# Optimization experiments

Hardware: AMD Instinct MI355X
Metric: run time of the kernel (lower is better)

The kernel has to match this reference:

```python
import jax, jax.numpy as jnp
import numpy as np

M, D, NI, L, NPL, R, T = 2, 128, 131072, 4, 2048, 8, 32
N = NI + L * NPL  # total DAG nodes


def setup_inputs() -> dict:
    key = jax.random.key(0)
    ks = jax.random.split(key, 18)
    thax = jax.random.randint(ks[0], (NI,), 0, T)
    sine = jax.random.uniform(ks[1], (NI,), jnp.float32)
    # parents of layer-l deriv nodes index any node built earlier (topological)
    raw = jax.random.randint(ks[2], (L, NPL, 2), 0, 2**30)
    bounds = jnp.array([NI + l * NPL for l in range(L)])[:, None, None]
    par = raw % bounds
    ridx = jax.random.randint(ks[3], (L, NPL), 0, R)
    pos = jax.random.uniform(ks[4], (N,), jnp.float32) + 0.01
    neg = jax.random.uniform(ks[5], (N,), jnp.float32) + 0.01
    s = 0.05
    return {
        'thax': thax, 'sine': sine, 'par': par, 'ridx': ridx,
        'pos': pos, 'neg': neg,
        'init_table': jax.random.normal(ks[6], (M, T, D)) * s,
        's_vec': jax.random.normal(ks[7], (M, D)) * s,
        'W1': jax.random.normal(ks[8], (M, R, 2 * D, D)) * s,
        'b1': jax.random.normal(ks[9], (M, R, D)) * s,
        'W2': jax.random.normal(ks[10], (M, R, D, D)) * s,
        'b2': jax.random.normal(ks[11], (M, R, D)) * s,
        'tweaks': jax.random.normal(ks[12], (M, 1, 2)) * s,
        'We1': jax.random.normal(ks[13], (M, D, D)) * s,
        'be1': jax.random.normal(ks[14], (M, D)) * s,
        'we2': jax.random.normal(ks[15], (M, D)) * s,
        'be2': jax.random.normal(ks[16], (M,)) * s,
    }


def reference(thax, sine, par, ridx, pos, neg, init_table, s_vec,
              W1, b1, W2, b2, tweaks, We1, be1, we2, be2):
    # init nodes: thax embedding + sine embellishment (per model)
    emb0 = init_table[:, thax, :] + sine[None, :, None] * s_vec[:, None, :]  # [M,NI,D]
    store = jnp.zeros((M, N, D), emb0.dtype).at[:, :NI].set(emb0)
    # topological layers of deriv nodes: gather parents, rule-indexed 2-layer MLP
    for l in range(L):
        p, r = par[l], ridx[l]
        cat = store[:, p].reshape(M, NPL, 2 * D)               # gather parents
        h = jax.nn.relu(jnp.einsum('mnc,mncd->mnd', cat, W1[:, r]) + b1[:, r])
        out = (jnp.einsum('mnd,mnde->mne', h, W2[:, r]) + b2[:, r]
               + tweaks[:, 0, 1][:, None, None])
        store = store.at[:, NI + l * NPL: NI + (l + 1) * NPL].set(out)
    # eval_net: per-node scalar logit (+ per-problem tweak)
    he = jax.nn.relu(jnp.einsum('mnd,mde->mne', store, We1) + be1[:, None, :])
    logit = jnp.einsum('mnd,md->mn', he, we2) + be2[:, None] + tweaks[:, 0, 0][:, None]
    tot_pos, tot_neg = pos.sum(), neg.sum()
    pw = tot_neg / tot_pos  # POS_WEIGHT_EXTRA = 1.0
    gold = pos / (pos + neg)
    w = pos + neg
    # BCEWithLogitsLoss(pos_weight=pw) per node, weighted by (pos+neg)
    bce = -(pw * gold[None] * jax.nn.log_sigmoid(logit)
            + (1.0 - gold[None]) * jax.nn.log_sigmoid(-logit))
    loss = (w[None] * bce).sum(axis=1)                          # [M]
    posOK = jnp.where(logit >= 0, pos[None], 0.0).sum(axis=1)
    negOK = jnp.where(logit < 0, neg[None], 0.0).sum(axis=1)
    return (loss, posOK, negOK, tot_pos, tot_neg)
```

## Files before the change

kernel.cpp:

```cpp
#include <hip/hip_runtime.h>
#include <hip/hip_bf16.h>

#define M_ 2
#define D_ 128
#define NI_ 131072
#define L_ 4
#define NPL_ 2048
#define R_ 8
#define T_ 32
#define N_ (NI_ + L_ * NPL_)
#define ND_ (L_ * NPL_)
#define PART2_ 1184

typedef __bf16 bf16x8 __attribute__((ext_vector_type(8)));
typedef float f32x4 __attribute__((ext_vector_type(4)));

#define OFF_W1T    0u
#define OFF_W2T    1048576u
#define OFF_WE1T   1572864u
#define OFF_TAB    1638400u
#define OFF_SVEC   1654784u
#define OFF_SORTED 1655296u
#define OFF_STARTS 1688064u
#define OFF_CNTF   1688192u
#define OFF_CNTA   1688320u
#define OFF_EA2    1688448u
#define OFF_EWB    1721216u
#define OFF_PA     1723264u
#define OFF_PB     1739648u
#define OFF_PPOK   1756032u
#define OFF_PNOK   1772416u
#define OFF_PTP    1788800u
#define OFF_PTN    1805184u
#define OFF_G      1821568u
#define OFF_STORE  2362240u
#define OFF_FSG    6556544u
#define OFF_CFG    6556576u
#define OFF_FLIST  6556608u
#define OFF_RDY    6589376u

__device__ __forceinline__ unsigned short f2bu(float f) {
  unsigned int u = __float_as_uint(f);
  u += 0x7fffu + ((u >> 16) & 1u);
  return (unsigned short)(u >> 16);
}
__device__ __forceinline__ bf16x8 ldb8(const unsigned short* p) {
  return *reinterpret_cast<const bf16x8*>(p);
}

__device__ __forceinline__ bf16x8 node_chunk(int m, int row, int d0,
    const unsigned short* tab, const unsigned short* svec,
    const unsigned short* sd, const int* thax, const float* sine) {
  if (row < NI_) {
    bf16x8 tv = ldb8(&tab[(m * T_ + thax[row]) * D_ + d0]);
    bf16x8 sv = ldb8(&svec[m * D_ + d0]);
    float sn = sine[row];
    bf16x8 r;
#pragma unroll
    for (int j = 0; j < 8; ++j)
      r[j] = (__bf16)((float)tv[j] + sn * (float)sv[j]);
    return r;
  }
  return ldb8(&sd[(size_t)(m * ND_ + (row - NI_)) * D_ + d0]);
}

__global__ __launch_bounds__(256) void megaprep_kernel(
    const float* W1, const float* W2, const float* We1,
    const float* init_table, const float* s_vec,
    const float* b1, const float* be1, const float* we2,
    const int* ridx, const int* par,
    unsigned short* W1T, unsigned short* W2T, unsigned short* We1T,
    unsigned short* tab, unsigned short* svec,
    float* G, float* EA2, float* EWB,
    int* sorted, int* starts, int* cntF, int* cntA,
    int* fsg, int* cfg, int* fastlist, unsigned int* rdy, unsigned int* pzero) {
  __shared__ float smem[1056];
  __shared__ int icnt[16], ioff[16];
  int job = blockIdx.x;
  int tid = threadIdx.x;

  if (job < 800) {
    int z, rblk, cblk;
    if (job < 512)      { z = job >> 5;            rblk = (job & 31) >> 2; cblk = job & 3; }
    else if (job < 768) { int q = job - 512; z = 16 + (q >> 4); rblk = (q & 15) >> 2; cblk = q & 3; }
    else                { int q = job - 768; z = 32 + (q >> 4); rblk = (q & 15) >> 2; cblk = q & 3; }
    const float* src; unsigned short* dst; int R;
    if (z < 16)      { src = W1  + (size_t)z * 32768;        dst = W1T  + (size_t)z * 32768;        R = 256; }
    else if (z < 32) { src = W2  + (size_t)(z - 16) * 16384; dst = W2T  + (size_t)(z - 16) * 16384; R = 128; }
    else             { src = We1 + (size_t)(z - 32) * 16384; dst = We1T + (size_t)(z - 32) * 16384; R = 128; }
    int r0 = rblk * 32, c0 = cblk * 32;
    float (*tile)[33] = (float(*)[33])smem;
    int tx = tid & 31, ty = tid >> 5;
#pragma unroll
    for (int k = 0; k < 4; ++k)
      tile[ty + 8 * k][tx] = src[(size_t)(r0 + ty + 8 * k) * D_ + c0 + tx];
    __syncthreads();
#pragma unroll
    for (int k = 0; k < 4; ++k)
      dst[(size_t)(c0 + ty + 8 * k) * R + r0 + tx] = f2bu(tile[tx][ty + 8 * k]);
  } else if (job == 800) {
    for (int i = tid; i < 8448; i += 256) {
      if (i < 8192) tab[i] = f2bu(init_table[i]);
      else svec[i - 8192] = f2bu(s_vec[i - 8192]);
    }
  } else if (job < 1329) {
    int q = job - 801;
    int t = q / 16, mr = q & 15;
    int m = mr >> 3;
    int slot = tid >> 7, e = tid & 127;
    const float* vec = (t < 32) ? &init_table[(size_t)(m * T_ + t) * D_]
                                : &s_vec[(size_t)m * D_];
    if (tid < 128) smem[tid] = vec[tid];
    __syncthreads();
    const float* w = &W1[((size_t)mr * 256 + slot * 128) * D_];
    float acc = 0.f;
#pragma unroll 8
    for (int c = 0; c < 128; ++c) acc = fmaf(smem[c], w[c * D_ + e], acc);
    if (slot == 0 && t < 32) acc += b1[mr * D_ + e];
    G[((size_t)(mr * 2 + slot) * 33 + t) * D_ + e] = acc;
  } else if (job < 1363) {
    int q = job - 1329;
    int m = q / 17, t = (q % 17) * 2 + (tid >> 7);
    int e = tid & 127;
    if (t <= 32) {
      const float* vec = (t < 32) ? &init_table[(size_t)(m * T_ + t) * D_]
                                  : &s_vec[(size_t)m * D_];
      const float* w = &We1[(size_t)m * D_ * D_];
      float acc = 0.f;
#pragma unroll 8
      for (int d = 0; d < 128; ++d) acc = fmaf(vec[d], w[d * D_ + e], acc);
      if (t < 32) {
        EA2[m * 4096 + ((e >> 1) * 32 + t) * 2 + (e & 1)] = acc + be1[m * D_ + e];
      } else {
        EWB[(m * D_ + e) * 2 + 0] = acc;
        EWB[(m * D_ + e) * 2 + 1] = we2[m * D_ + e];
      }
    }
  } else if (job < 1367) {
    int l = job - 1363;
    if (tid < 16) icnt[tid] = 0;
    __syncthreads();
    for (int n = tid; n < NPL_; n += 256) {
      int r = ridx[l * NPL_ + n];
      int p0 = par[(l * NPL_ + n) * 2 + 0], p1 = par[(l * NPL_ + n) * 2 + 1];
      int slow = (p0 >= NI_ || p1 >= NI_) ? 1 : 0;
      atomicAdd(&icnt[r * 2 + slow], 1);
    }
    __syncthreads();
    if (tid == 0) {
      int run = 0;
      for (int b = 0; b < 16; ++b) { ioff[b] = run; run += icnt[b]; }
      for (int r = 0; r < R_; ++r) {
        starts[l * R_ + r] = ioff[2 * r];
        cntF[l * R_ + r] = icnt[2 * r];
        cntA[l * R_ + r] = icnt[2 * r] + icnt[2 * r + 1];
      }
    }
    __syncthreads();
    for (int n = tid; n < NPL_; n += 256) {
      int r = ridx[l * NPL_ + n];
      int p0 = par[(l * NPL_ + n) * 2 + 0], p1 = par[(l * NPL_ + n) * 2 + 1];
      int slow = (p0 >= NI_ || p1 >= NI_) ? 1 : 0;
      int p = atomicAdd(&ioff[r * 2 + slow], 1);
      sorted[l * NPL_ + p] = n;
    }
  } else if (job == 1367) {
    if (tid < 8) icnt[tid] = 0;
    __syncthreads();
    for (int g = tid; g < ND_; g += 256) {
      int p0 = par[2 * g], p1 = par[2 * g + 1];
      int fast = (p0 < NI_ && p1 < NI_) ? 1 : 0;
      if (fast) atomicAdd(&icnt[ridx[g]], 1);
      rdy[g] = fast ? 2u : 0u;
      rdy[ND_ + g] = fast ? 2u : 0u;
    }
    __syncthreads();
    if (tid == 0) {
      int run = 0;
      for (int r = 0; r < R_; ++r) {
        ioff[r] = run; fsg[r] = run; cfg[r] = icnt[r]; run += icnt[r];
      }
    }
    __syncthreads();
    for (int g = tid; g < ND_; g += 256) {
      int p0 = par[2 * g], p1 = par[2 * g + 1];
      if (p0 < NI_ && p1 < NI_) {
        int p = atomicAdd(&ioff[ridx[g]], 1);
        fastlist[p] = g;
      }
    }
  } else {
    for (int i = tid; i < 24576; i += 256) pzero[i] = 0u;
  }
}

__global__ __launch_bounds__(256) void main_kernel(
    const int* thax, const float* sine, const int* par,
    const float* pos, const float* neg,
    const float* b2, const float* tweaks,
    const float* G, const unsigned short* W2T, const unsigned short* We1T,
    const float* EA2, const float* EWB,
    const float* be1, const float* we2, const float* be2,
    const int* fsg, const int* cfg, const int* fastlist,
    unsigned short* sd,
    float* pA, float* pB, float* pPok, float* pNok, float* pTp, float* pTn) {
  __shared__ float sbuf[4448];
  int bid = blockIdx.x;
  int tid = threadIdx.x;
  int w = tid >> 6, lane = tid & 63;

  if (bid < 1280) {
    int m = bid / 640, q = bid % 640;
    int r = q / 80, tile = q % 80;
    int cnt = cfg[r];
    int base = tile * 16;
    if (base >= cnt) return;
    unsigned short* h_lds = (unsigned short*)sbuf;
    int*   t0a  = (int*)(sbuf + 1024);
    int*   t1a  = t0a + 16;
    float* s0a  = (float*)(t1a + 16);
    float* s1a  = s0a + 16;
    int*   gida = (int*)(s1a + 16);
    float* red2 = sbuf + 1104;
    if (tid < 16) {
      int loc = base + tid; if (loc >= cnt) loc = cnt - 1;
      int gid = fastlist[fsg[r] + loc];
      int p0 = par[2 * gid], p1 = par[2 * gid + 1];
      t0a[tid] = thax[p0]; s0a[tid] = sine[p0];
      t1a[tid] = thax[p1]; s1a[tid] = sine[p1];
      gida[tid] = gid;
    }
    __syncthreads();
    const float* Gm = &G[(size_t)(m * R_ + r) * 8448];
    {
      int row = tid >> 4, seg = tid & 15, d0 = seg * 8;
      int t0 = t0a[row], t1 = t1a[row];
      float s0 = s0a[row], s1 = s1a[row];
      const float* pa = &Gm[t0 * 128 + d0];
      const float* pb = &Gm[(33 + t1) * 128 + d0];
      const float* pu = &Gm[4096 + d0];
      const float* pv = &Gm[8320 + d0];
      bf16x8 hv;
#pragma unroll
      for (int half = 0; half < 2; ++half) {
        float4 a = *(const float4*)(pa + half * 4);
        float4 b = *(const float4*)(pb + half * 4);
        float4 u = *(const float4*)(pu + half * 4);
        float4 v = *(const float4*)(pv + half * 4);
        hv[half * 4 + 0] = (__bf16)fmaxf(a.x + b.x + s0 * u.x + s1 * v.x, 0.f);
        hv[half * 4 + 1] = (__bf16)fmaxf(a.y + b.y + s0 * u.y + s1 * v.y, 0.f);
        hv[half * 4 + 2] = (__bf16)fmaxf(a.z + b.z + s0 * u.z + s1 * v.z, 0.f);
        hv[half * 4 + 3] = (__bf16)fmaxf(a.w + b.w + s0 * u.w + s1 * v.w, 0.f);
      }
      *(bf16x8*)&h_lds[row * 128 + (d0 ^ ((row & 7) << 3))] = hv;
    }
    __syncthreads();
    int l15 = lane & 15, l4 = lane >> 4;
    const unsigned short* w2b = &W2T[(size_t)(m * R_ + r) * D_ * D_];
    f32x4 acc[2];
    acc[0] = (f32x4){0.f, 0.f, 0.f, 0.f};
    acc[1] = (f32x4){0.f, 0.f, 0.f, 0.f};
#pragma unroll
    for (int kc = 0; kc < 4; ++kc) {
      int d0 = kc * 32 + l4 * 8;
      bf16x8 a2 = ldb8(&h_lds[l15 * 128 + (d0 ^ ((l15 & 7) << 3))]);
#pragma unroll
      for (int f = 0; f < 2; ++f) {
        int fg = w * 2 + f;
        bf16x8 b = ldb8(&w2b[(fg * 16 + l15) * D_ + d0]);
        acc[f] = __builtin_amdgcn_mfma_f32_16x16x32_bf16(a2, b, acc[f], 0, 0, 0);
      }
    }
    float tw1 = tweaks[m * 2 + 1];
    const float* b2v = &b2[(m * R_ + r) * D_];
    __syncthreads();
#pragma unroll
    for (int i = 0; i < 4; ++i) {
      int row = l4 * 4 + i;
      int g = base + row;
#pragma unroll
      for (int f = 0; f < 2; ++f) {
        int e = (w * 2 + f) * 16 + l15;
        unsigned short val = f2bu(acc[f][i] + b2v[e] + tw1);
        h_lds[row * 128 + (e ^ ((row & 7) << 3))] = val;
        if (g < cnt) sd[(size_t)(m * ND_ + gida[row]) * D_ + e] = val;
      }
    }
    __syncthreads();
    f32x4 ae[2];
    ae[0] = (f32x4){0.f, 0.f, 0.f, 0.f};
    ae[1] = (f32x4){0.f, 0.f, 0.f, 0.f};
    const unsigned short* we1b = &We1T[(size_t)m * D_ * D_];
#pragma unroll
    for (int kc = 0; kc < 4; ++kc) {
      int d0 = kc * 32 + l4 * 8;
      bf16x8 a2 = ldb8(&h_lds[l15 * 128 + (d0 ^ ((l15 & 7) << 3))]);
#pragma unroll
      for (int f = 0; f < 2; ++f) {
        int fg = w * 2 + f;
        bf16x8 b = ldb8(&we1b[(fg * 16 + l15) * D_ + d0]);
        ae[f] = __builtin_amdgcn_mfma_f32_16x16x32_bf16(a2, b, ae[f], 0, 0, 0);
      }
    }
    float part[4] = {0.f, 0.f, 0.f, 0.f};
#pragma unroll
    for (int f = 0; f < 2; ++f) {
      int e = (w * 2 + f) * 16 + l15;
      float bb = be1[m * D_ + e];
      float wv = we2[m * D_ + e];
#pragma unroll
      for (int i = 0; i < 4; ++i) {
        float he = ae[f][i] + bb;
        he = he > 0.f ? he : 0.f;
        part[i] += he * wv;
      }
    }
#pragma unroll
    for (int mask = 1; mask < 16; mask <<= 1) {
#pragma unroll
      for (int i = 0; i < 4; ++i) part[i] += __shfl_xor(part[i], mask, 64);
    }
    if (l15 == 0) {
#pragma unroll
      for (int i = 0; i < 4; ++i) red2[w * 16 + l4 * 4 + i] = part[i];
    }
    __syncthreads();
    if (tid < 16) {
      int g = base + tid;
      float v6[6] = {0.f, 0.f, 0.f, 0.f, 0.f, 0.f};
      if (g < cnt) {
        float logit = red2[tid] + red2[16 + tid] + red2[32 + tid] + red2[48 + tid]
                    + be2[m] + tweaks[m * 2 + 0];
        int grow = NI_ + gida[tid];
        float p_ = pos[grow], n_ = neg[grow];
        float lse = log1pf(__expf(-fabsf(logit)));
        v6[0] = p_ * (fmaxf(-logit, 0.f) + lse);
        v6[1] = n_ * (fmaxf(logit, 0.f) + lse);
        v6[2] = logit >= 0.f ? p_ : 0.f;
        v6[3] = logit < 0.f ? n_ : 0.f;
        v6[4] = p_; v6[5] = n_;
      }
#pragma unroll
      for (int mask = 1; mask < 16; mask <<= 1) {
#pragma unroll
        for (int qq = 0; qq < 6; ++qq) v6[qq] += __shfl_xor(v6[qq], mask, 64);
      }
      if (tid == 0) {
        int slot = 512 + r * 80 + tile;
        pA[m * PART2_ + slot] = v6[0];
        pB[m * PART2_ + slot] = v6[1];
        pPok[m * PART2_ + slot] = v6[2];
        pNok[m * PART2_ + slot] = v6[3];
        if (m == 0) { pTp[slot] = v6[4]; pTn[slot] = v6[5]; }
      }
    }
  } else {
    int q = bid - 1280;
    int m = q >> 9, xb = q & 511;
    float* lea = sbuf;
    float* lwb = sbuf + 4096;
    float* red = sbuf + 4352;
    for (int i = tid; i < 4096; i += 256) lea[i] = EA2[m * 4096 + i];
    if (tid < 256) lwb[tid] = EWB[m * 256 + tid];
    __syncthreads();
    int row = xb * 256 + tid;
    int t = thax[row];
    float s = sine[row];
    float acc = 0.f;
#pragma unroll 8
    for (int p = 0; p < 64; ++p) {
      float2 ea = *(const float2*)&lea[(p * 32 + t) * 2];
      float4 wb = *(const float4*)&lwb[p * 4];
      float x0 = fmaf(s, wb.x, ea.x); x0 = fmaxf(x0, 0.f);
      acc = fmaf(x0, wb.y, acc);
      float x1 = fmaf(s, wb.z, ea.y); x1 = fmaxf(x1, 0.f);
      acc = fmaf(x1, wb.w, acc);
    }
    float logit = acc + be2[m] + tweaks[m * 2 + 0];
    float p_ = pos[row], n_ = neg[row];
    float lse = log1pf(__expf(-fabsf(logit)));
    float v[6];
    v[0] = p_ * (fmaxf(-logit, 0.f) + lse);
    v[1] = n_ * (fmaxf(logit, 0.f) + lse);
    v[2] = logit >= 0.f ? p_ : 0.f;
    v[3] = logit < 0.f ? n_ : 0.f;
    v[4] = p_; v[5] = n_;
#pragma unroll
    for (int mask = 1; mask < 64; mask <<= 1) {
#pragma unroll
      for (int k = 0; k < 6; ++k) v[k] += __shfl_xor(v[k], mask, 64);
    }
    if (lane == 0) {
#pragma unroll
      for (int k = 0; k < 6; ++k) red[k * 16 + w] = v[k];
    }
    __syncthreads();
    if (tid == 0) {
      float t6[6];
#pragma unroll
      for (int k = 0; k < 6; ++k)
        t6[k] = red[k * 16 + 0] + red[k * 16 + 1] + red[k * 16 + 2] + red[k * 16 + 3];
      pA[m * PART2_ + xb] = t6[0];
      pB[m * PART2_ + xb] = t6[1];
      pPok[m * PART2_ + xb] = t6[2];
      pNok[m * PART2_ + xb] = t6[3];
      if (m == 0) { pTp[xb] = t6[4]; pTn[xb] = t6[5]; }
    }
  }
}

__global__ __launch_bounds__(256) void slowfused_kernel(
    const int* thax, const float* sine, const int* par,
    const float* b1, const float* b2, const float* tweaks,
    const float* pos, const float* neg,
    const float* be1, const float* we2, const float* be2,
    const unsigned short* tab, const unsigned short* svec,
    const unsigned short* W1T, const unsigned short* W2T,
    const unsigned short* We1T,
    const int* sorted, const int* starts, const int* cntF, const int* cntA,
    unsigned short* sd, unsigned int* rdy,
    float* pA, float* pB, float* pPok, float* pNok, float* pTp, float* pTn) {
  __shared__ unsigned short h_lds[16 * 128];
  __shared__ float red2[64];
  __shared__ float pacc[6];
  __shared__ int sfl;
  int bid = blockIdx.x;
  int m = bid >> 5, r = (bid >> 2) & 7, ts = bid & 3;
  int tid = threadIdx.x;
  int w = tid >> 6, lane = tid & 63;
  int l15 = lane & 15, l4 = lane >> 4;
  if (tid < 6) pacc[tid] = 0.f;
  float tw1 = tweaks[m * 2 + 1];
  const float* b2v = &b2[(m * R_ + r) * D_];
  const unsigned short* w1b = &W1T[(size_t)(m * R_ + r) * D_ * 256];
  const unsigned short* w2b = &W2T[(size_t)(m * R_ + r) * D_ * D_];
  const unsigned short* we1b = &We1T[(size_t)m * D_ * D_];

  for (int l = 1; l < L_; ++l) {
    int cF = cntF[l * R_ + r];
    int cS = cntA[l * R_ + r] - cF;
    int base = ts * 16;
    if (base < cS) {
      int start = starts[l * R_ + r] + cF;
      if (tid == 0) sfl = 0;
      __syncthreads();
      if (tid < 32) {
        int row = tid >> 1, which = tid & 1;
        int loc = base + row; if (loc >= cS) loc = cS - 1;
        int node = sorted[l * NPL_ + start + loc];
        int p = par[(l * NPL_ + node) * 2 + which];
        if (p >= NI_) {
          unsigned int* fp = &rdy[(size_t)m * ND_ + (p - NI_)];
          unsigned int v = __hip_atomic_load(fp, __ATOMIC_ACQUIRE, __HIP_MEMORY_SCOPE_AGENT);
          int spins = 0;
          while (v == 0 && spins < (1 << 17)) {
            __builtin_amdgcn_s_sleep(8);
            v = __hip_atomic_load(fp, __ATOMIC_ACQUIRE, __HIP_MEMORY_SCOPE_AGENT);
            ++spins;
          }
          if (v != 2u) atomicOr(&sfl, 1);
        }
      }
      __syncthreads();
      if (sfl && tid == 0) __threadfence();
      __syncthreads();
      int loc = base + l15; if (loc >= cS) loc = cS - 1;
      int node = sorted[l * NPL_ + start + loc];
      int p0 = par[(l * NPL_ + node) * 2 + 0];
      int p1 = par[(l * NPL_ + node) * 2 + 1];
      bf16x8 av[8];
#pragma unroll
      for (int kc = 0; kc < 8; ++kc) {
        int k = kc * 32 + l4 * 8;
        int p = (k < 128) ? p0 : p1;
        av[kc] = node_chunk(m, p, k & 127, tab, svec, sd, thax, sine);
      }
      f32x4 acch[2];
      acch[0] = (f32x4){0.f, 0.f, 0.f, 0.f};
      acch[1] = (f32x4){0.f, 0.f, 0.f, 0.f};
#pragma unroll
      for (int kc = 0; kc < 8; ++kc) {
        int k = kc * 32 + l4 * 8;
#pragma unroll
        for (int f = 0; f < 2; ++f) {
          int fg = w * 2 + f;
          bf16x8 b = ldb8(&w1b[(fg * 16 + l15) * 256 + k]);
          acch[f] = __builtin_amdgcn_mfma_f32_16x16x32_bf16(av[kc], b, acch[f], 0, 0, 0);
        }
      }
      const float* b1v = &b1[(m * R_ + r) * D_];
#pragma unroll
      for (int f = 0; f < 2; ++f) {
        int d = (w * 2 + f) * 16 + l15;
        float bb = b1v[d];
#pragma unroll
        for (int i = 0; i < 4; ++i) {
          int row = l4 * 4 + i;
          float h = acch[f][i] + bb;
          h = h > 0.f ? h : 0.f;
          h_lds[row * 128 + (d ^ ((row & 7) << 3))] = f2bu(h);
        }
      }
      __syncthreads();
      f32x4 acco[2];
      acco[0] = (f32x4){0.f, 0.f, 0.f, 0.f};
      acco[1] = (f32x4){0.f, 0.f, 0.f, 0.f};
#pragma unroll
      for (int kc = 0; kc < 4; ++kc) {
        int d0 = kc * 32 + l4 * 8;
        bf16x8 a2 = ldb8(&h_lds[l15 * 128 + (d0 ^ ((l15 & 7) << 3))]);
#pragma unroll
        for (int f = 0; f < 2; ++f) {
          int fg = w * 2 + f;
          bf16x8 b = ldb8(&w2b[(fg * 16 + l15) * D_ + d0]);
          acco[f] = __builtin_amdgcn_mfma_f32_16x16x32_bf16(a2, b, acco[f], 0, 0, 0);
        }
      }
      __syncthreads();
#pragma unroll
      for (int i = 0; i < 4; ++i) {
        int row = l4 * 4 + i;
        int g = base + row;
#pragma unroll
        for (int f = 0; f < 2; ++f) {
          int e = (w * 2 + f) * 16 + l15;
          unsigned short val = f2bu(acco[f][i] + b2v[e] + tw1);
          h_lds[row * 128 + (e ^ ((row & 7) << 3))] = val;
          if (g < cS) {
            int nd = sorted[l * NPL_ + start + g];
            sd[(size_t)(m * ND_ + l * NPL_ + nd) * D_ + e] = val;
          }
        }
      }
      __syncthreads();
      if (tid == 0) __threadfence();
      __syncthreads();
      if (tid < 16) {
        int g = base + tid;
        if (g < cS) {
          int nd = sorted[l * NPL_ + start + g];
          __hip_atomic_store(&rdy[(size_t)m * ND_ + l * NPL_ + nd], 1u,
                             __ATOMIC_RELAXED, __HIP_MEMORY_SCOPE_AGENT);
        }
      }
      f32x4 ae[2];
      ae[0] = (f32x4){0.f, 0.f, 0.f, 0.f};
      ae[1] = (f32x4){0.f, 0.f, 0.f, 0.f};
#pragma unroll
      for (int kc = 0; kc < 4; ++kc) {
        int d0 = kc * 32 + l4 * 8;
        bf16x8 a2 = ldb8(&h_lds[l15 * 128 + (d0 ^ ((l15 & 7) << 3))]);
#pragma unroll
        for (int f = 0; f < 2; ++f) {
          int fg = w * 2 + f;
          bf16x8 b = ldb8(&we1b[(fg * 16 + l15) * D_ + d0]);
          ae[f] = __builtin_amdgcn_mfma_f32_16x16x32_bf16(a2, b, ae[f], 0, 0, 0);
        }
      }
      float part[4] = {0.f, 0.f, 0.f, 0.f};
#pragma unroll
      for (int f = 0; f < 2; ++f) {
        int e = (w * 2 + f) * 16 + l15;
        float bb = be1[m * D_ + e];
        float wv = we2[m * D_ + e];
#pragma unroll
        for (int i = 0; i < 4; ++i) {
          float he = ae[f][i] + bb;
          he = he > 0.f ? he : 0.f;
          part[i] += he * wv;
        }
      }
#pragma unroll
      for (int mask = 1; mask < 16; mask <<= 1) {
#pragma unroll
        for (int i = 0; i < 4; ++i) part[i] += __shfl_xor(part[i], mask, 64);
      }
      if (l15 == 0) {
#pragma unroll
        for (int i = 0; i < 4; ++i) red2[w * 16 + l4 * 4 + i] = part[i];
      }
      __syncthreads();
      if (tid < 16) {
        int g = base + tid;
        float v6[6] = {0.f, 0.f, 0.f, 0.f, 0.f, 0.f};
        if (g < cS) {
          float logit = red2[tid] + red2[16 + tid] + red2[32 + tid] + red2[48 + tid]
                      + be2[m] + tweaks[m * 2 + 0];
          int nd = sorted[l * NPL_ + start + g];
          int grow = NI_ + l * NPL_ + nd;
          float p_ = pos[grow], n_ = neg[grow];
          float lse = log1pf(__expf(-fabsf(logit)));
          v6[0] = p_ * (fmaxf(-logit, 0.f) + lse);
          v6[1] = n_ * (fmaxf(logit, 0.f) + lse);
          v6[2] = logit >= 0.f ? p_ : 0.f;
          v6[3] = logit < 0.f ? n_ : 0.f;
          v6[4] = p_; v6[5] = n_;
        }
#pragma unroll
        for (int mask = 1; mask < 16; mask <<= 1) {
#pragma unroll
          for (int qq = 0; qq < 6; ++qq) v6[qq] += __shfl_xor(v6[qq], mask, 64);
        }
        if (tid == 0) {
#pragma unroll
          for (int qq = 0; qq < 6; ++qq) pacc[qq] += v6[qq];
        }
      }
      __syncthreads();
    }
  }
  if (tid == 0) {
    int slot = 1152 + (r * 4 + ts);
    pA[m * PART2_ + slot] = pacc[0];
    pB[m * PART2_ + slot] = pacc[1];
    pPok[m * PART2_ + slot] = pacc[2];
    pNok[m * PART2_ + slot] = pacc[3];
    if (m == 0) { pTp[slot] = pacc[4]; pTn[slot] = pacc[5]; }
  }
}

__global__ __launch_bounds__(256) void finalize_kernel(
    const float* pA, const float* pB, const float* pPok, const float* pNok,
    const float* pTp, const float* pTn, float* out) {
  __shared__ float lred[10][4];
  const float* srcs[10] = {pA, pA + PART2_, pB, pB + PART2_,
                           pPok, pPok + PART2_, pNok, pNok + PART2_,
                           pTp, pTn};
  int tid = threadIdx.x;
  int w = tid >> 6, lane = tid & 63;
#pragma unroll
  for (int q = 0; q < 10; ++q) {
    float s = 0.f;
    for (int i = tid; i < PART2_; i += 256) s += srcs[q][i];
#pragma unroll
    for (int mask = 1; mask < 64; mask <<= 1) s += __shfl_xor(s, mask, 64);
    if (lane == 0) lred[q][w] = s;
  }
  __syncthreads();
  if (tid == 0) {
    float totals[10];
#pragma unroll
    for (int q = 0; q < 10; ++q)
      totals[q] = lred[q][0] + lred[q][1] + lred[q][2] + lred[q][3];
    float tp = totals[8], tn = totals[9];
    float pw = tn / tp;
    out[0] = pw * totals[0] + totals[2];
    out[1] = pw * totals[1] + totals[3];
    out[2] = totals[4]; out[3] = totals[5];
    out[4] = totals[6]; out[5] = totals[7];
    out[6] = tp; out[7] = tn;
  }
}

extern "C" void kernel_launch(void* const* d_in, const int* in_sizes, int n_in,
                              void* d_out, int out_size, void* d_ws, size_t ws_size,
                              hipStream_t stream) {
  const int*   thax = (const int*)d_in[0];
  const float* sine = (const float*)d_in[1];
  const int*   par  = (const int*)d_in[2];
  const int*   ridx = (const int*)d_in[3];
  const float* pos  = (const float*)d_in[4];
  const float* neg  = (const float*)d_in[5];
  const float* init_table = (const float*)d_in[6];
  const float* s_vec = (const float*)d_in[7];
  const float* W1 = (const float*)d_in[8];
  const float* b1 = (const float*)d_in[9];
  const float* W2 = (const float*)d_in[10];
  const float* b2 = (const float*)d_in[11];
  const float* tweaks = (const float*)d_in[12];
  const float* We1 = (const float*)d_in[13];
  const float* be1 = (const float*)d_in[14];
  const float* we2 = (const float*)d_in[15];
  const float* be2 = (const float*)d_in[16];

  char* ws = (char*)d_ws;
  unsigned short* W1T  = (unsigned short*)(ws + OFF_W1T);
  unsigned short* W2T  = (unsigned short*)(ws + OFF_W2T);
  unsigned short* We1T = (unsigned short*)(ws + OFF_WE1T);
  unsigned short* tab  = (unsigned short*)(ws + OFF_TAB);
  unsigned short* svec = (unsigned short*)(ws + OFF_SVEC);
  int* sorted = (int*)(ws + OFF_SORTED);
  int* starts = (int*)(ws + OFF_STARTS);
  int* cntF   = (int*)(ws + OFF_CNTF);
  int* cntA   = (int*)(ws + OFF_CNTA);
  float* EA2  = (float*)(ws + OFF_EA2);
  float* EWB  = (float*)(ws + OFF_EWB);
  float* pA   = (float*)(ws + OFF_PA);
  float* pB   = (float*)(ws + OFF_PB);
  float* pPok = (float*)(ws + OFF_PPOK);
  float* pNok = (float*)(ws + OFF_PNOK);
  float* pTp  = (float*)(ws + OFF_PTP);
  float* pTn  = (float*)(ws + OFF_PTN);
  float* G    = (float*)(ws + OFF_G);
  unsigned short* sd = (unsigned short*)(ws + OFF_STORE);
  int* fsg      = (int*)(ws + OFF_FSG);
  int* cfg      = (int*)(ws + OFF_CFG);
  int* fastlist = (int*)(ws + OFF_FLIST);
  unsigned int* rdy = (unsigned int*)(ws + OFF_RDY);

  megaprep_kernel<<<1369, 256, 0, stream>>>(
      W1, W2, We1, init_table, s_vec, b1, be1, we2, ridx, par,
      W1T, W2T, We1T, tab, svec, G, EA2, EWB, sorted, starts, cntF, cntA,
      fsg, cfg, fastlist, rdy, (unsigned int*)pA);
  main_kernel<<<2304, 256, 0, stream>>>(
      thax, sine, par, pos, neg, b2, tweaks, G, W2T, We1T, EA2, EWB,
      be1, we2, be2, fsg, cfg, fastlist, sd,
      pA, pB, pPok, pNok, pTp, pTn);
  slowfused_kernel<<<64, 256, 0, stream>>>(
      thax, sine, par, b1, b2, tweaks, pos, neg, be1, we2, be2,
      tab, svec, W1T, W2T, We1T, sorted, starts, cntF, cntA,
      sd, rdy, pA, pB, pPok, pNok, pTp, pTn);
  finalize_kernel<<<1, 256, 0, stream>>>(pA, pB, pPok, pNok, pTp, pTn,
                                         (float*)d_out);
}
```

Before: 102.1 us.

## Replace spin-wait ready flags with per-layer kernel launches for slow nodes

The persistent slow-path kernel, which used per-node ready flags with acquire spin loops to enforce cross-layer dependencies, is replaced by three launches of a slow-node kernel, one per layer (layers 1-3). Each launch uses a grid of 8 tiles by 8 rules by 2 models with 128-thread blocks, and each wave computes four 16-column groups. This removes the rdy array initialization, the spin polling and the fences, and lets the launch boundary provide the ordering. The cost is two extra kernel launches, and each layer now runs with a fixed grid in which blocks past the slow-node count exit early.

```diff
diff --git a/kernel.cpp b/kernel.cpp
--- a/kernel.cpp
+++ b/kernel.cpp
@@ -10,7 +10,7 @@
 #define T_ 32
 #define N_ (NI_ + L_ * NPL_)
 #define ND_ (L_ * NPL_)
-#define PART2_ 1184
+#define PART3_ 1344
 
 typedef __bf16 bf16x8 __attribute__((ext_vector_type(8)));
 typedef float f32x4 __attribute__((ext_vector_type(4)));
@@ -27,17 +27,16 @@
 #define OFF_EA2    1688448u
 #define OFF_EWB    1721216u
 #define OFF_PA     1723264u
-#define OFF_PB     1739648u
-#define OFF_PPOK   1756032u
-#define OFF_PNOK   1772416u
-#define OFF_PTP    1788800u
-#define OFF_PTN    1805184u
-#define OFF_G      1821568u
-#define OFF_STORE  2362240u
-#define OFF_FSG    6556544u
-#define OFF_CFG    6556576u
-#define OFF_FLIST  6556608u
-#define OFF_RDY    6589376u
+#define OFF_PB     1734016u
+#define OFF_PPOK   1744768u
+#define OFF_PNOK   1755520u
+#define OFF_PTP    1766272u
+#define OFF_PTN    1771648u
+#define OFF_G      1777024u
+#define OFF_STORE  2317696u
+#define OFF_FSG    6512000u
+#define OFF_CFG    6512032u
+#define OFF_FLIST  6512064u
 
 __device__ __forceinline__ unsigned short f2bu(float f) {
   unsigned int u = __float_as_uint(f);
@@ -73,7 +72,7 @@
     unsigned short* tab, unsigned short* svec,
     float* G, float* EA2, float* EWB,
     int* sorted, int* starts, int* cntF, int* cntA,
-    int* fsg, int* cfg, int* fastlist, unsigned int* rdy, unsigned int* pzero) {
+    int* fsg, int* cfg, int* fastlist, unsigned int* pzero) {
   __shared__ float smem[1056];
   __shared__ int icnt[16], ioff[16];
   int job = blockIdx.x;
@@ -169,10 +168,7 @@
     __syncthreads();
     for (int g = tid; g < ND_; g += 256) {
       int p0 = par[2 * g], p1 = par[2 * g + 1];
-      int fast = (p0 < NI_ && p1 < NI_) ? 1 : 0;
-      if (fast) atomicAdd(&icnt[ridx[g]], 1);
-      rdy[g] = fast ? 2u : 0u;
-      rdy[ND_ + g] = fast ? 2u : 0u;
+      if (p0 < NI_ && p1 < NI_) atomicAdd(&icnt[ridx[g]], 1);
     }
     __syncthreads();
     if (tid == 0) {
@@ -190,7 +186,7 @@
       }
     }
   } else {
-    for (int i = tid; i < 24576; i += 256) pzero[i] = 0u;
+    for (int i = tid; i < 13440; i += 256) pzero[i] = 0u;
   }
 }
 
@@ -347,10 +343,10 @@
       }
       if (tid == 0) {
         int slot = 512 + r * 80 + tile;
-        pA[m * PART2_ + slot] = v6[0];
-        pB[m * PART2_ + slot] = v6[1];
-        pPok[m * PART2_ + slot] = v6[2];
-        pNok[m * PART2_ + slot] = v6[3];
+        pA[m * PART3_ + slot] = v6[0];
+        pB[m * PART3_ + slot] = v6[1];
+        pPok[m * PART3_ + slot] = v6[2];
+        pNok[m * PART3_ + slot] = v6[3];
         if (m == 0) { pTp[slot] = v6[4]; pTn[slot] = v6[5]; }
       }
     }
@@ -400,16 +396,16 @@
 #pragma unroll
       for (int k = 0; k < 6; ++k)
         t6[k] = red[k * 16 + 0] + red[k * 16 + 1] + red[k * 16 + 2] + red[k * 16 + 3];
-      pA[m * PART2_ + xb] = t6[0];
-      pB[m * PART2_ + xb] = t6[1];
-      pPok[m * PART2_ + xb] = t6[2];
-      pNok[m * PART2_ + xb] = t6[3];
+      pA[m * PART3_ + xb] = t6[0];
+      pB[m * PART3_ + xb] = t6[1];
+      pPok[m * PART3_ + xb] = t6[2];
+      pNok[m * PART3_ + xb] = t6[3];
       if (m == 0) { pTp[xb] = t6[4]; pTn[xb] = t6[5]; }
     }
   }
 }
 
-__global__ __launch_bounds__(256) void slowfused_kernel(
+__global__ __launch_bounds__(128) void slow_eval_kernel(int l,
     const int* thax, const float* sine, const int* par,
     const float* b1, const float* b2, const float* tweaks,
     const float* pos, const float* neg,
@@ -418,204 +414,160 @@
     const unsigned short* W1T, const unsigned short* W2T,
     const unsigned short* We1T,
     const int* sorted, const int* starts, const int* cntF, const int* cntA,
-    unsigned short* sd, unsigned int* rdy,
+    unsigned short* sd,
     float* pA, float* pB, float* pPok, float* pNok, float* pTp, float* pTn) {
-  __shared__ unsigned short h_lds[16 * 128];
-  __shared__ float red2[64];
-  __shared__ float pacc[6];
-  __shared__ int sfl;
-  int bid = blockIdx.x;
-  int m = bid >> 5, r = (bid >> 2) & 7, ts = bid & 3;
+  int tile = blockIdx.x, r = blockIdx.y, m = blockIdx.z;
+  int cF = cntF[l * R_ + r];
+  int cS = cntA[l * R_ + r] - cF;
+  int base = tile * 16;
+  if (base >= cS) return;
+  int start = starts[l * R_ + r] + cF;
   int tid = threadIdx.x;
   int w = tid >> 6, lane = tid & 63;
   int l15 = lane & 15, l4 = lane >> 4;
-  if (tid < 6) pacc[tid] = 0.f;
-  float tw1 = tweaks[m * 2 + 1];
-  const float* b2v = &b2[(m * R_ + r) * D_];
+  __shared__ unsigned short h_lds[16 * 128];
+  __shared__ float red2[32];
+
+  int loc = base + l15; if (loc >= cS) loc = cS - 1;
+  int node = sorted[l * NPL_ + start + loc];
+  int p0 = par[(l * NPL_ + node) * 2 + 0];
+  int p1 = par[(l * NPL_ + node) * 2 + 1];
   const unsigned short* w1b = &W1T[(size_t)(m * R_ + r) * D_ * 256];
   const unsigned short* w2b = &W2T[(size_t)(m * R_ + r) * D_ * D_];
   const unsigned short* we1b = &We1T[(size_t)m * D_ * D_];
 
-  for (int l = 1; l < L_; ++l) {
-    int cF = cntF[l * R_ + r];
-    int cS = cntA[l * R_ + r] - cF;
-    int base = ts * 16;
-    if (base < cS) {
-      int start = starts[l * R_ + r] + cF;
-      if (tid == 0) sfl = 0;
-      __syncthreads();
-      if (tid < 32) {
-        int row = tid >> 1, which = tid & 1;
-        int loc = base + row; if (loc >= cS) loc = cS - 1;
-        int node = sorted[l * NPL_ + start + loc];
-        int p = par[(l * NPL_ + node) * 2 + which];
-        if (p >= NI_) {
-          unsigned int* fp = &rdy[(size_t)m * ND_ + (p - NI_)];
-          unsigned int v = __hip_atomic_load(fp, __ATOMIC_ACQUIRE, __HIP_MEMORY_SCOPE_AGENT);
-          int spins = 0;
-          while (v == 0 && spins < (1 << 17)) {
-            __builtin_amdgcn_s_sleep(8);
-            v = __hip_atomic_load(fp, __ATOMIC_ACQUIRE, __HIP_MEMORY_SCOPE_AGENT);
-            ++spins;
-          }
-          if (v != 2u) atomicOr(&sfl, 1);
-        }
-      }
-      __syncthreads();
-      if (sfl && tid == 0) __threadfence();
-      __syncthreads();
-      int loc = base + l15; if (loc >= cS) loc = cS - 1;
-      int node = sorted[l * NPL_ + start + loc];
-      int p0 = par[(l * NPL_ + node) * 2 + 0];
-      int p1 = par[(l * NPL_ + node) * 2 + 1];
-      bf16x8 av[8];
-#pragma unroll
-      for (int kc = 0; kc < 8; ++kc) {
-        int k = kc * 32 + l4 * 8;
-        int p = (k < 128) ? p0 : p1;
-        av[kc] = node_chunk(m, p, k & 127, tab, svec, sd, thax, sine);
-      }
-      f32x4 acch[2];
-      acch[0] = (f32x4){0.f, 0.f, 0.f, 0.f};
-      acch[1] = (f32x4){0.f, 0.f, 0.f, 0.f};
-#pragma unroll
-      for (int kc = 0; kc < 8; ++kc) {
-        int k = kc * 32 + l4 * 8;
-#pragma unroll
-        for (int f = 0; f < 2; ++f) {
-          int fg = w * 2 + f;
-          bf16x8 b = ldb8(&w1b[(fg * 16 + l15) * 256 + k]);
-          acch[f] = __builtin_amdgcn_mfma_f32_16x16x32_bf16(av[kc], b, acch[f], 0, 0, 0);
-        }
-      }
-      const float* b1v = &b1[(m * R_ + r) * D_];
-#pragma unroll
-      for (int f = 0; f < 2; ++f) {
-        int d = (w * 2 + f) * 16 + l15;
-        float bb = b1v[d];
-#pragma unroll
-        for (int i = 0; i < 4; ++i) {
-          int row = l4 * 4 + i;
-          float h = acch[f][i] + bb;
-          h = h > 0.f ? h : 0.f;
-          h_lds[row * 128 + (d ^ ((row & 7) << 3))] = f2bu(h);
-        }
-      }
-      __syncthreads();
-      f32x4 acco[2];
-      acco[0] = (f32x4){0.f, 0.f, 0.f, 0.f};
-      acco[1] = (f32x4){0.f, 0.f, 0.f, 0.f};
-#pragma unroll
-      for (int kc = 0; kc < 4; ++kc) {
-        int d0 = kc * 32 + l4 * 8;
-        bf16x8 a2 = ldb8(&h_lds[l15 * 128 + (d0 ^ ((l15 & 7) << 3))]);
-#pragma unroll
-        for (int f = 0; f < 2; ++f) {
-          int fg = w * 2 + f;
-          bf16x8 b = ldb8(&w2b[(fg * 16 + l15) * D_ + d0]);
-          acco[f] = __builtin_amdgcn_mfma_f32_16x16x32_bf16(a2, b, acco[f], 0, 0, 0);
-        }
-      }
-      __syncthreads();
-#pragma unroll
-      for (int i = 0; i < 4; ++i) {
-        int row = l4 * 4 + i;
-        int g = base + row;
-#pragma unroll
-        for (int f = 0; f < 2; ++f) {
-          int e = (w * 2 + f) * 16 + l15;
-          unsigned short val = f2bu(acco[f][i] + b2v[e] + tw1);
-          h_lds[row * 128 + (e ^ ((row & 7) << 3))] = val;
-          if (g < cS) {
-            int nd = sorted[l * NPL_ + start + g];
-            sd[(size_t)(m * ND_ + l * NPL_ + nd) * D_ + e] = val;
-          }
-        }
-      }
-      __syncthreads();
-      if (tid == 0) __threadfence();
-      __syncthreads();
-      if (tid < 16) {
-        int g = base + tid;
-        if (g < cS) {
-          int nd = sorted[l * NPL_ + start + g];
-          __hip_atomic_store(&rdy[(size_t)m * ND_ + l * NPL_ + nd], 1u,
-                             __ATOMIC_RELAXED, __HIP_MEMORY_SCOPE_AGENT);
-        }
-      }
-      f32x4 ae[2];
-      ae[0] = (f32x4){0.f, 0.f, 0.f, 0.f};
-      ae[1] = (f32x4){0.f, 0.f, 0.f, 0.f};
-#pragma unroll
-      for (int kc = 0; kc < 4; ++kc) {
-        int d0 = kc * 32 + l4 * 8;
-        bf16x8 a2 = ldb8(&h_lds[l15 * 128 + (d0 ^ ((l15 & 7) << 3))]);
-#pragma unroll
-        for (int f = 0; f < 2; ++f) {
-          int fg = w * 2 + f;
-          bf16x8 b = ldb8(&we1b[(fg * 16 + l15) * D_ + d0]);
-          ae[f] = __builtin_amdgcn_mfma_f32_16x16x32_bf16(a2, b, ae[f], 0, 0, 0);
-        }
-      }
-      float part[4] = {0.f, 0.f, 0.f, 0.f};
-#pragma unroll
-      for (int f = 0; f < 2; ++f) {
-        int e = (w * 2 + f) * 16 + l15;
-        float bb = be1[m * D_ + e];
-        float wv = we2[m * D_ + e];
-#pragma unroll
-        for (int i = 0; i < 4; ++i) {
-          float he = ae[f][i] + bb;
-          he = he > 0.f ? he : 0.f;
-          part[i] += he * wv;
-        }
-      }
-#pragma unroll
-      for (int mask = 1; mask < 16; mask <<= 1) {
-#pragma unroll
-        for (int i = 0; i < 4; ++i) part[i] += __shfl_xor(part[i], mask, 64);
-      }
-      if (l15 == 0) {
-#pragma unroll
-        for (int i = 0; i < 4; ++i) red2[w * 16 + l4 * 4 + i] = part[i];
-      }
-      __syncthreads();
-      if (tid < 16) {
-        int g = base + tid;
-        float v6[6] = {0.f, 0.f, 0.f, 0.f, 0.f, 0.f};
-        if (g < cS) {
-          float logit = red2[tid] + red2[16 + tid] + red2[32 + tid] + red2[48 + tid]
-                      + be2[m] + tweaks[m * 2 + 0];
-          int nd = sorted[l * NPL_ + start + g];
-          int grow = NI_ + l * NPL_ + nd;
-          float p_ = pos[grow], n_ = neg[grow];
-          float lse = log1pf(__expf(-fabsf(logit)));
-          v6[0] = p_ * (fmaxf(-logit, 0.f) + lse);
-          v6[1] = n_ * (fmaxf(logit, 0.f) + lse);
-          v6[2] = logit >= 0.f ? p_ : 0.f;
-          v6[3] = logit < 0.f ? n_ : 0.f;
-          v6[4] = p_; v6[5] = n_;
-        }
-#pragma unroll
-        for (int mask = 1; mask < 16; mask <<= 1) {
-#pragma unroll
-          for (int qq = 0; qq < 6; ++qq) v6[qq] += __shfl_xor(v6[qq], mask, 64);
-        }
-        if (tid == 0) {
-#pragma unroll
-          for (int qq = 0; qq < 6; ++qq) pacc[qq] += v6[qq];
-        }
-      }
-      __syncthreads();
-    }
-  }
-  if (tid == 0) {
-    int slot = 1152 + (r * 4 + ts);
-    pA[m * PART2_ + slot] = pacc[0];
-    pB[m * PART2_ + slot] = pacc[1];
-    pPok[m * PART2_ + slot] = pacc[2];
-    pNok[m * PART2_ + slot] = pacc[3];
-    if (m == 0) { pTp[slot] = pacc[4]; pTn[slot] = pacc[5]; }
+  bf16x8 av[8];
+#pragma unroll
+  for (int kc = 0; kc < 8; ++kc) {
+    int k = kc * 32 + l4 * 8;
+    int p = (k < 128) ? p0 : p1;
+    av[kc] = node_chunk(m, p, k & 127, tab, svec, sd, thax, sine);
+  }
+  f32x4 acch[4];
+#pragma unroll
+  for (int f = 0; f < 4; ++f) acch[f] = (f32x4){0.f, 0.f, 0.f, 0.f};
+#pragma unroll
+  for (int kc = 0; kc < 8; ++kc) {
+    int k = kc * 32 + l4 * 8;
+#pragma unroll
+    for (int f = 0; f < 4; ++f) {
+      int fg = w * 4 + f;
+      bf16x8 b = ldb8(&w1b[(fg * 16 + l15) * 256 + k]);
+      acch[f] = __builtin_amdgcn_mfma_f32_16x16x32_bf16(av[kc], b, acch[f], 0, 0, 0);
+    }
+  }
+  const float* b1v = &b1[(m * R_ + r) * D_];
+#pragma unroll
+  for (int f = 0; f < 4; ++f) {
+    int d = (w * 4 + f) * 16 + l15;
+    float bb = b1v[d];
+#pragma unroll
+    for (int i = 0; i < 4; ++i) {
+      int row = l4 * 4 + i;
+      float h = acch[f][i] + bb;
+      h = h > 0.f ? h : 0.f;
+      h_lds[row * 128 + (d ^ ((row & 7) << 3))] = f2bu(h);
+    }
+  }
+  __syncthreads();
+  f32x4 acco[4];
+#pragma unroll
+  for (int f = 0; f < 4; ++f) acco[f] = (f32x4){0.f, 0.f, 0.f, 0.f};
+#pragma unroll
+  for (int kc = 0; kc < 4; ++kc) {
+    int d0 = kc * 32 + l4 * 8;
+    bf16x8 a2 = ldb8(&h_lds[l15 * 128 + (d0 ^ ((l15 & 7) << 3))]);
+#pragma unroll
+    for (int f = 0; f < 4; ++f) {
+      int fg = w * 4 + f;
+      bf16x8 b = ldb8(&w2b[(fg * 16 + l15) * D_ + d0]);
+      acco[f] = __builtin_amdgcn_mfma_f32_16x16x32_bf16(a2, b, acco[f], 0, 0, 0);
+    }
+  }
+  float tw1 = tweaks[m * 2 + 1];
+  const float* b2v = &b2[(m * R_ + r) * D_];
+  __syncthreads();
+#pragma unroll
+  for (int i = 0; i < 4; ++i) {
+    int row = l4 * 4 + i;
+    int g = base + row;
+#pragma unroll
+    for (int f = 0; f < 4; ++f) {
+      int e = (w * 4 + f) * 16 + l15;
+      unsigned short val = f2bu(acco[f][i] + b2v[e] + tw1);
+      h_lds[row * 128 + (e ^ ((row & 7) << 3))] = val;
+      if (g < cS) {
+        int nd = sorted[l * NPL_ + start + g];
+        sd[(size_t)(m * ND_ + l * NPL_ + nd) * D_ + e] = val;
+      }
+    }
+  }
+  __syncthreads();
+  f32x4 ae[4];
+#pragma unroll
+  for (int f = 0; f < 4; ++f) ae[f] = (f32x4){0.f, 0.f, 0.f, 0.f};
+#pragma unroll
+  for (int kc = 0; kc < 4; ++kc) {
+    int d0 = kc * 32 + l4 * 8;
+    bf16x8 a2 = ldb8(&h_lds[l15 * 128 + (d0 ^ ((l15 & 7) << 3))]);
+#pragma unroll
+    for (int f = 0; f < 4; ++f) {
+      int fg = w * 4 + f;
+      bf16x8 b = ldb8(&we1b[(fg * 16 + l15) * D_ + d0]);
+      ae[f] = __builtin_amdgcn_mfma_f32_16x16x32_bf16(a2, b, ae[f], 0, 0, 0);
+    }
+  }
+  float part[4] = {0.f, 0.f, 0.f, 0.f};
+#pragma unroll
+  for (int f = 0; f < 4; ++f) {
+    int e = (w * 4 + f) * 16 + l15;
+    float bb = be1[m * D_ + e];
+    float wv = we2[m * D_ + e];
+#pragma unroll
+    for (int i = 0; i < 4; ++i) {
+      float he = ae[f][i] + bb;
+      he = he > 0.f ? he : 0.f;
+      part[i] += he * wv;
+    }
+  }
+#pragma unroll
+  for (int mask = 1; mask < 16; mask <<= 1) {
+#pragma unroll
+    for (int i = 0; i < 4; ++i) part[i] += __shfl_xor(part[i], mask, 64);
+  }
+  if (l15 == 0) {
+#pragma unroll
+    for (int i = 0; i < 4; ++i) red2[w * 16 + l4 * 4 + i] = part[i];
+  }
+  __syncthreads();
+  if (tid < 16) {
+    int g = base + tid;
+    float v6[6] = {0.f, 0.f, 0.f, 0.f, 0.f, 0.f};
+    if (g < cS) {
+      float logit = red2[tid] + red2[16 + tid] + be2[m] + tweaks[m * 2 + 0];
+      int nd = sorted[l * NPL_ + start + g];
+      int grow = NI_ + l * NPL_ + nd;
+      float p_ = pos[grow], n_ = neg[grow];
+      float lse = log1pf(__expf(-fabsf(logit)));
+      v6[0] = p_ * (fmaxf(-logit, 0.f) + lse);
+      v6[1] = n_ * (fmaxf(logit, 0.f) + lse);
+      v6[2] = logit >= 0.f ? p_ : 0.f;
+      v6[3] = logit < 0.f ? n_ : 0.f;
+      v6[4] = p_; v6[5] = n_;
+    }
+#pragma unroll
+    for (int mask = 1; mask < 16; mask <<= 1) {
+#pragma unroll
+      for (int qq = 0; qq < 6; ++qq) v6[qq] += __shfl_xor(v6[qq], mask, 64);
+    }
+    if (tid == 0) {
+      int slot = 1152 + (l - 1) * 64 + r * 8 + tile;
+      pA[m * PART3_ + slot] = v6[0];
+      pB[m * PART3_ + slot] = v6[1];
+      pPok[m * PART3_ + slot] = v6[2];
+      pNok[m * PART3_ + slot] = v6[3];
+      if (m == 0) { pTp[slot] = v6[4]; pTn[slot] = v6[5]; }
+    }
   }
 }
 
@@ -623,15 +575,15 @@
     const float* pA, const float* pB, const float* pPok, const float* pNok,
     const float* pTp, const float* pTn, float* out) {
   __shared__ float lred[10][4];
-  const float* srcs[10] = {pA, pA + PART2_, pB, pB + PART2_,
-                           pPok, pPok + PART2_, pNok, pNok + PART2_,
+  const float* srcs[10] = {pA, pA + PART3_, pB, pB + PART3_,
+                           pPok, pPok + PART3_, pNok, pNok + PART3_,
                            pTp, pTn};
   int tid = threadIdx.x;
   int w = tid >> 6, lane = tid & 63;
 #pragma unroll
   for (int q = 0; q < 10; ++q) {
     float s = 0.f;
-    for (int i = tid; i < PART2_; i += 256) s += srcs[q][i];
+    for (int i = tid; i < PART3_; i += 256) s += srcs[q][i];
 #pragma unroll
     for (int mask = 1; mask < 64; mask <<= 1) s += __shfl_xor(s, mask, 64);
     if (lane == 0) lred[q][w] = s;
@@ -696,20 +648,21 @@
   int* fsg      = (int*)(ws + OFF_FSG);
   int* cfg      = (int*)(ws + OFF_CFG);
   int* fastlist = (int*)(ws + OFF_FLIST);
-  unsigned int* rdy = (unsigned int*)(ws + OFF_RDY);
 
   megaprep_kernel<<<1369, 256, 0, stream>>>(
       W1, W2, We1, init_table, s_vec, b1, be1, we2, ridx, par,
       W1T, W2T, We1T, tab, svec, G, EA2, EWB, sorted, starts, cntF, cntA,
-      fsg, cfg, fastlist, rdy, (unsigned int*)pA);
+      fsg, cfg, fastlist, (unsigned int*)pA);
   main_kernel<<<2304, 256, 0, stream>>>(
       thax, sine, par, pos, neg, b2, tweaks, G, W2T, We1T, EA2, EWB,
       be1, we2, be2, fsg, cfg, fastlist, sd,
       pA, pB, pPok, pNok, pTp, pTn);
-  slowfused_kernel<<<64, 256, 0, stream>>>(
-      thax, sine, par, b1, b2, tweaks, pos, neg, be1, we2, be2,
-      tab, svec, W1T, W2T, We1T, sorted, starts, cntF, cntA,
-      sd, rdy, pA, pB, pPok, pNok, pTp, pTn);
+  for (int l = 1; l < L_; ++l) {
+    slow_eval_kernel<<<dim3(8, R_, M_), 128, 0, stream>>>(
+        l, thax, sine, par, b1, b2, tweaks, pos, neg, be1, we2, be2,
+        tab, svec, W1T, W2T, We1T, sorted, starts, cntF, cntA, sd,
+        pA, pB, pPok, pNok, pTp, pTn);
+  }
   finalize_kernel<<<1, 256, 0, stream>>>(pA, pB, pPok, pNok, pTp, pTn,
                                          (float*)d_out);
 }
```

Result: no change. 100.7 us (-1.4%).
